# Kernel tuning notes

Measured on AMD Instinct MI355X. Metric: run time of the kernel, lower is better.

Reference implementation:

```python
import jax, jax.numpy as jnp
import numpy as np

N_QUBITS = 12
FEATURE_DIM = 512
BATCH = 8192


def setup_inputs() -> dict:
    key = jax.random.key(0)
    k1, k2, k3 = jax.random.split(key, 3)
    x = jax.random.normal(k1, (BATCH, FEATURE_DIM), dtype=jnp.float32)
    W = jax.random.normal(k2, (N_QUBITS * 3, FEATURE_DIM), dtype=jnp.float32) * 0.05
    b = jax.random.normal(k3, (N_QUBITS * 3,), dtype=jnp.float32) * 0.05
    return {"x": x, "W": W, "b": b}


def _simulate(angles):
    """Batched analytic state-vector simulation.
    angles: (B, n, 3) rotation angles (RX, RY, RZ) per qubit.
    Circuit: per-qubit RX->RY->RZ on |0>, then CNOT chain (q -> q+1),
    then <Z_q> for each qubit. Wire 0 is the most significant bit
    (PennyLane default.qubit convention).
    """
    B, n, _ = angles.shape
    half = angles * 0.5
    a, be, g = half[..., 0], half[..., 1], half[..., 2]  # (B, n) each
    # RX(a)|0> = [cos(a/2), -i sin(a/2)]
    u0 = jnp.cos(a).astype(jnp.complex64)
    u1 = (-1j) * jnp.sin(a).astype(jnp.complex64)
    # RY(b) applied: [[c,-s],[s,c]]
    cb, sb = jnp.cos(be), jnp.sin(be)
    w0 = cb * u0 - sb * u1
    w1 = sb * u0 + cb * u1
    # RZ(g): diag(e^{-i g/2}, e^{+i g/2})
    ph = jnp.exp((-1j) * g.astype(jnp.complex64))
    s0 = w0 * ph
    s1 = w1 * jnp.conj(ph)
    qvecs = jnp.stack([s0, s1], axis=-1)  # (B, n, 2) single-qubit states

    # Product state via iterative kron: (B, 2^n), qubit 0 most significant.
    state = qvecs[:, 0, :]
    for q in range(1, n):
        state = (state[:, :, None] * qvecs[:, q, None, :]).reshape(B, -1)

    # CNOT chain on adjacent wires (q control, q+1 target).
    for q in range(n - 1):
        s = state.reshape(B, 2 ** q, 2, 2, -1)  # (B, lead, ctrl, tgt, rest)
        c0 = s[:, :, 0]
        c1 = s[:, :, 1, ::-1]  # flip target amplitudes when control = 1
        state = jnp.stack([c0, c1], axis=2).reshape(B, -1)

    probs = state.real ** 2 + state.imag ** 2  # (B, 2^n), float32
    # <Z_q> = sum_i probs[i] * (1 - 2*bit_q(i)), bit of wire q is MSB-first.
    idx = np.arange(2 ** n, dtype=np.int64)
    bits = (idx[:, None] >> np.arange(n - 1, -1, -1)[None, :]) & 1
    signs = jnp.asarray(1.0 - 2.0 * bits, dtype=jnp.float32)  # (2^n, n)
    return probs @ signs  # (B, n)


def reference(x, W, b):
    angles = (x @ W.T + b).reshape(x.shape[0], N_QUBITS, 3)
    return _simulate(angles)
```

## Files before the change

kernel.cpp:

```cpp
#include <hip/hip_runtime.h>


#define NQ    12
#define NDOT  24
#define KDIM  512
#define ROWS_PER_BLOCK 16

__global__ __launch_bounds__(256, 2) void qgate_kernel(
    const float* __restrict__ x,
    const float* __restrict__ W,
    const float* __restrict__ b,
    float* __restrict__ out)
{
    __shared__ float4 wlds[NDOT * 128];

    const int tid = threadIdx.x;
    for (int i = tid; i < NDOT * 128; i += 256) {
        const int d  = i >> 7;
        const int kk = i & 127;
        const int r  = (d >> 1) * 3 + (d & 1);
        wlds[i] = reinterpret_cast<const float4*>(W)[r * 128 + kk];
    }
    __syncthreads();

    const int l    = tid & 31;
    const int g    = tid >> 5;
    const int row0 = blockIdx.x * ROWS_PER_BLOCK + g * 2;

    const float4* __restrict__ xp0 =
        reinterpret_cast<const float4*>(x + (size_t)row0 * KDIM);
    const float4* __restrict__ xp1 =
        reinterpret_cast<const float4*>(x + (size_t)(row0 + 1) * KDIM);

    float4 xv0[4], xv1[4];
#pragma unroll
    for (int c = 0; c < 4; ++c) { xv0[c] = xp0[c * 32 + l]; xv1[c] = xp1[c * 32 + l]; }

    float2 a0[NDOT], a1[NDOT];
#pragma unroll
    for (int d = 0; d < NDOT; ++d) {
        a0[d] = make_float2(0.f, 0.f);
        a1[d] = make_float2(0.f, 0.f);
    }

#pragma unroll
    for (int c = 0; c < 4; ++c) {
#pragma unroll
        for (int d = 0; d < NDOT; ++d) {
            const float4 wv = wlds[d * 128 + c * 32 + l];
            a0[d].x = fmaf(xv0[c].x, wv.x, a0[d].x);
            a0[d].y = fmaf(xv0[c].y, wv.y, a0[d].y);
            a0[d].x = fmaf(xv0[c].z, wv.z, a0[d].x);
            a0[d].y = fmaf(xv0[c].w, wv.w, a0[d].y);
            a1[d].x = fmaf(xv1[c].x, wv.x, a1[d].x);
            a1[d].y = fmaf(xv1[c].y, wv.y, a1[d].y);
            a1[d].x = fmaf(xv1[c].z, wv.z, a1[d].x);
            a1[d].y = fmaf(xv1[c].w, wv.w, a1[d].y);
        }
    }

    const bool hi = (l & 16) != 0;
    float v[32];
#pragma unroll
    for (int d = 0; d < NDOT; ++d) {
        const float s0d = a0[d].x + a0[d].y;
        const float s1d = a1[d].x + a1[d].y;
        const float mine  = hi ? s1d : s0d;
        const float send  = hi ? s0d : s1d;
        v[d] = mine + __shfl_xor(send, 16);
    }
#pragma unroll
    for (int d = NDOT; d < 32; ++d) v[d] = 0.f;

    float u16[16];
#pragma unroll
    for (int i = 0; i < 16; ++i) {
        const float keep = (l & 8) ? v[16 + i] : v[i];
        const float send = (l & 8) ? v[i] : v[16 + i];
        u16[i] = keep + __shfl_xor(send, 8);
    }
    float u8[8];
#pragma unroll
    for (int i = 0; i < 8; ++i) {
        const float keep = (l & 4) ? u16[8 + i] : u16[i];
        const float send = (l & 4) ? u16[i] : u16[8 + i];
        u8[i] = keep + __shfl_xor(send, 4);
    }
    float u4[4];
#pragma unroll
    for (int i = 0; i < 4; ++i) {
        const float keep = (l & 2) ? u8[4 + i] : u8[i];
        const float send = (l & 2) ? u8[i] : u8[4 + i];
        u4[i] = keep + __shfl_xor(send, 2);
    }
    float u2[2];
#pragma unroll
    for (int i = 0; i < 2; ++i) {
        const float keep = (l & 1) ? u4[2 + i] : u4[i];
        const float send = (l & 1) ? u4[i] : u4[2 + i];
        u2[i] = keep + __shfl_xor(send, 1);
    }

    const int j  = l & 15;
    const int jc = (j < NQ) ? j : NQ - 1;
    const float aj = u2[0] + b[3 * jc];
    const float bj = u2[1] + b[3 * jc + 1];
    float p = __cosf(aj) * __cosf(bj);

#pragma unroll
    for (int st = 1; st < 16; st <<= 1) {
        const float t = __shfl_up(p, st, 16);
        if (j >= st) p *= t;
    }

    if (j < NQ) out[(size_t)(row0 + (hi ? 1 : 0)) * NQ + j] = p;
}

extern "C" void kernel_launch(void* const* d_in, const int* in_sizes, int n_in,
                              void* d_out, int out_size, void* d_ws, size_t ws_size,
                              hipStream_t stream) {
    const float* x = (const float*)d_in[0];
    const float* W = (const float*)d_in[1];
    const float* b = (const float*)d_in[2];
    float* out     = (float*)d_out;

    const int batch = in_sizes[0] / KDIM;
    const int grid  = batch / ROWS_PER_BLOCK;
    qgate_kernel<<<grid, 256, 0, stream>>>(x, W, b, out);
}
```

Baseline: 74.01 us.

## Process four rows per full wavefront to halve LDS weight reads per row

Each 64-lane wavefront now computes four batch rows instead of each 32-lane half-wave computing two. Every lane covers two float4 chunks of K, so each weight value loaded from LDS feeds four rows' FMAs instead of two. The cross-lane reduction gains an extra xor-32 shuffle stage, and the output row index is derived from lane bits 4-5. This raises the accumulator count to 96 registers per lane, which increases register pressure.

```diff
diff --git a/kernel.cpp b/kernel.cpp
--- a/kernel.cpp
+++ b/kernel.cpp
@@ -23,60 +23,67 @@
     }
     __syncthreads();
 
-    const int l    = tid & 31;
-    const int g    = tid >> 5;
-    const int row0 = blockIdx.x * ROWS_PER_BLOCK + g * 2;
+    const int l    = tid & 63;
+    const int w    = tid >> 6;
+    const int row0 = blockIdx.x * ROWS_PER_BLOCK + w * 4;
 
-    const float4* __restrict__ xp0 =
-        reinterpret_cast<const float4*>(x + (size_t)row0 * KDIM);
-    const float4* __restrict__ xp1 =
-        reinterpret_cast<const float4*>(x + (size_t)(row0 + 1) * KDIM);
-
-    float4 xv0[4], xv1[4];
+    float4 xv[4][2];
 #pragma unroll
-    for (int c = 0; c < 4; ++c) { xv0[c] = xp0[c * 32 + l]; xv1[c] = xp1[c * 32 + l]; }
-
-    float2 a0[NDOT], a1[NDOT];
+    for (int r = 0; r < 4; ++r) {
+        const float4* __restrict__ xp =
+            reinterpret_cast<const float4*>(x + (size_t)(row0 + r) * KDIM);
 #pragma unroll
-    for (int d = 0; d < NDOT; ++d) {
-        a0[d] = make_float2(0.f, 0.f);
-        a1[d] = make_float2(0.f, 0.f);
+        for (int c = 0; c < 2; ++c) xv[r][c] = xp[c * 64 + l];
     }
 
+    float acc[4][NDOT];
 #pragma unroll
-    for (int c = 0; c < 4; ++c) {
+    for (int r = 0; r < 4; ++r)
+#pragma unroll
+        for (int d = 0; d < NDOT; ++d) acc[r][d] = 0.f;
+
+#pragma unroll
+    for (int c = 0; c < 2; ++c) {
 #pragma unroll
         for (int d = 0; d < NDOT; ++d) {
-            const float4 wv = wlds[d * 128 + c * 32 + l];
-            a0[d].x = fmaf(xv0[c].x, wv.x, a0[d].x);
-            a0[d].y = fmaf(xv0[c].y, wv.y, a0[d].y);
-            a0[d].x = fmaf(xv0[c].z, wv.z, a0[d].x);
-            a0[d].y = fmaf(xv0[c].w, wv.w, a0[d].y);
-            a1[d].x = fmaf(xv1[c].x, wv.x, a1[d].x);
-            a1[d].y = fmaf(xv1[c].y, wv.y, a1[d].y);
-            a1[d].x = fmaf(xv1[c].z, wv.z, a1[d].x);
-            a1[d].y = fmaf(xv1[c].w, wv.w, a1[d].y);
+            const float4 wv = wlds[d * 128 + c * 64 + l];
+#pragma unroll
+            for (int r = 0; r < 4; ++r) {
+                acc[r][d] = fmaf(xv[r][c].x, wv.x, acc[r][d]);
+                acc[r][d] = fmaf(xv[r][c].y, wv.y, acc[r][d]);
+                acc[r][d] = fmaf(xv[r][c].z, wv.z, acc[r][d]);
+                acc[r][d] = fmaf(xv[r][c].w, wv.w, acc[r][d]);
+            }
         }
     }
 
-    const bool hi = (l & 16) != 0;
-    float v[32];
+    const bool h32 = (l & 32) != 0;
+    float vA[2][NDOT];
+#pragma unroll
+    for (int r = 0; r < 2; ++r)
+#pragma unroll
+        for (int d = 0; d < NDOT; ++d) {
+            const float keep = h32 ? acc[2 + r][d] : acc[r][d];
+            const float send = h32 ? acc[r][d]     : acc[2 + r][d];
+            vA[r][d] = keep + __shfl_xor(send, 32);
+        }
+
+    const bool h16 = (l & 16) != 0;
+    float v32[32];
 #pragma unroll
     for (int d = 0; d < NDOT; ++d) {
-        const float s0d = a0[d].x + a0[d].y;
-        const float s1d = a1[d].x + a1[d].y;
-        const float mine  = hi ? s1d : s0d;
-        const float send  = hi ? s0d : s1d;
-        v[d] = mine + __shfl_xor(send, 16);
+        const float keep = h16 ? vA[1][d] : vA[0][d];
+        const float send = h16 ? vA[0][d] : vA[1][d];
+        v32[d] = keep + __shfl_xor(send, 16);
     }
 #pragma unroll
-    for (int d = NDOT; d < 32; ++d) v[d] = 0.f;
+    for (int d = NDOT; d < 32; ++d) v32[d] = 0.f;
 
     float u16[16];
 #pragma unroll
     for (int i = 0; i < 16; ++i) {
-        const float keep = (l & 8) ? v[16 + i] : v[i];
-        const float send = (l & 8) ? v[i] : v[16 + i];
+        const float keep = (l & 8) ? v32[16 + i] : v32[i];
+        const float send = (l & 8) ? v32[i] : v32[16 + i];
         u16[i] = keep + __shfl_xor(send, 8);
     }
     float u8[8];
@@ -113,7 +120,7 @@
         if (j >= st) p *= t;
     }
 
-    if (j < NQ) out[(size_t)(row0 + (hi ? 1 : 0)) * NQ + j] = p;
+    if (j < NQ) out[(size_t)(row0 + ((l >> 4) & 3)) * NQ + j] = p;
 }
 
 extern "C" void kernel_launch(void* const* d_in, const int* in_sizes, int n_in,
```

Result: no change. 74.50 us (+0.7%).
